# Optimization experiments

Hardware: AMD Instinct MI355X
Metric: run time of the kernel (lower is better)

## Reference

```python
import jax, jax.numpy as jnp
import numpy as np

DIM = 1024
D_STATE = 16
D_CONV = 4
EXPAND = 2
D_INNER = EXPAND * DIM          # 2048
DT_RANK = -(-DIM // 16)        # ceil(dim/16) = 64
BATCH = 2
SEQ = 1024


def activation_quant(x):
    # int8 fake-quant with STE, per-row scale (matches torch source incl. grad paths)
    scale = 127.0 / jnp.clip(jnp.max(jnp.abs(x), axis=-1, keepdims=True), 1e-5)
    s = x * scale
    q = jnp.clip(jnp.round(s), -128.0, 127.0)
    return (jax.lax.stop_gradient(q - s) + s) / scale


def weight_quant(w):
    # ternary quant {-1,0,1} with straight-through estimator (grad = identity)
    scale = jnp.clip(jnp.mean(jnp.abs(w)), 1e-5)
    wq = jnp.clip(jnp.round(w / scale), -1.0, 1.0)
    return w + jax.lax.stop_gradient(wq - w)


def bit_linear(x, w):
    # LayerNorm (no affine, eps=1e-5) -> act quant -> ternary-weight matmul
    mu = jnp.mean(x, axis=-1, keepdims=True)
    var = jnp.mean((x - mu) ** 2, axis=-1, keepdims=True)
    xn = (x - mu) * jax.lax.rsqrt(var + 1e-5)
    return activation_quant(xn) @ weight_quant(w).T


def rms_norm(x, w, eps=1e-6):
    return w * (x * jax.lax.rsqrt(jnp.mean(x * x, axis=-1, keepdims=True) + eps))


def selective_scan(x, delta, A, Bm, Cm, D, z):
    # x, delta: [b,l,d]; Bm, Cm: [b,l,n]; A: [d,n]; D: [d]; z: [b,l,d]
    def step(h, inp):
        x_t, d_t, B_t, C_t = inp              # [b,d],[b,d],[b,n],[b,n]
        dA = jnp.exp(d_t[:, :, None] * A)     # [b,d,n]
        h = dA * h + d_t[:, :, None] * B_t[:, None, :] * x_t[:, :, None]
        y = jnp.einsum('bdn,bn->bd', h, C_t)
        return h, y

    h0 = jnp.zeros((x.shape[0], A.shape[0], A.shape[1]), x.dtype)
    seq_first = lambda t: jnp.moveaxis(t, 1, 0)
    _, ys = jax.lax.scan(step, h0, (seq_first(x), seq_first(delta), seq_first(Bm), seq_first(Cm)))
    y = jnp.moveaxis(ys, 0, 1) + x * D
    return y * jax.nn.silu(z)


def mamba_forward(hidden_states, rms_w, in_proj_w, x_proj_w, out_proj_w,
                  conv_w, conv_b, dt_proj_w, dt_proj_b, A_log, D):
    b, l, _ = hidden_states.shape
    h = rms_norm(hidden_states, rms_w)
    xz = bit_linear(h, in_proj_w)                      # [b,l,2*d_inner]
    x, z = jnp.split(xz, 2, axis=-1)

    # depthwise causal conv1d + bias
    xc = jnp.moveaxis(x, 1, 2)                         # [b,d_inner,l]
    xc = jax.lax.conv_general_dilated(
        xc, conv_w, window_strides=(1,), padding=[(D_CONV - 1, 0)],
        feature_group_count=D_INNER, dimension_numbers=('NCH', 'OIH', 'NCH'))
    xc = xc + conv_b[None, :, None]
    x = jax.nn.silu(jnp.moveaxis(xc, 1, 2))            # [b,l,d_inner]

    x_dbl = bit_linear(x, x_proj_w)                    # [b,l,dt_rank+2*d_state]
    dt_low, Bm, Cm = jnp.split(x_dbl, [DT_RANK, DT_RANK + D_STATE], axis=-1)
    dt = dt_low @ dt_proj_w.T + dt_proj_b              # dt_proj (with bias)
    # source passes dt_bias=dt_proj.bias again into the fused scan with softplus
    delta = jax.nn.softplus(dt + dt_proj_b)
    A = -jnp.exp(A_log)

    y = selective_scan(x, delta, A, Bm, Cm, D, z)
    out = bit_linear(y, out_proj_w)
    return hidden_states + out


def setup_inputs() -> dict:
    key = jax.random.key(0)
    ks = jax.random.split(key, 8)
    return {
        'hidden_states': jax.random.normal(ks[0], (BATCH, SEQ, DIM), jnp.float32),
        'rms_w': jnp.ones((DIM,), jnp.float32),
        'in_proj_w': jax.random.normal(ks[1], (2 * D_INNER, DIM), jnp.float32) / np.float32(np.sqrt(DIM)),
        'x_proj_w': jax.random.normal(ks[2], (DT_RANK + 2 * D_STATE, D_INNER), jnp.float32) / np.float32(np.sqrt(D_INNER)),
        'out_proj_w': jax.random.normal(ks[3], (DIM, D_INNER), jnp.float32) / np.float32(np.sqrt(D_INNER)),
        'conv_w': jax.random.normal(ks[4], (D_INNER, 1, D_CONV), jnp.float32) * 0.2,
        'conv_b': jnp.zeros((D_INNER,), jnp.float32),
        'dt_proj_w': jax.random.normal(ks[5], (D_INNER, DT_RANK), jnp.float32) / np.float32(np.sqrt(DT_RANK)),
        'dt_proj_b': jax.random.normal(ks[6], (D_INNER,), jnp.float32) * 0.01,
        'A_log': jnp.log(jnp.tile(jnp.arange(1, D_STATE + 1, dtype=jnp.float32), (D_INNER, 1))),
        'D': jnp.ones((D_INNER,), jnp.float32),
    }


def reference(hidden_states, rms_w, in_proj_w, x_proj_w, out_proj_w,
              conv_w, conv_b, dt_proj_w, dt_proj_b, A_log, D):
    return mamba_forward(hidden_states, rms_w, in_proj_w, x_proj_w, out_proj_w,
                         conv_w, conv_b, dt_proj_w, dt_proj_b, A_log, D)
```

## Files before the change

kernel.cpp:

```cpp
#include <hip/hip_runtime.h>
#include <hip/hip_bf16.h>

#define BATCH 2
#define SEQ 1024
#define DIM 1024
#define DINNER 2048
#define NSTATE 16
#define DTRANK 64
#define NDBL 96
#define ROWS (BATCH*SEQ)
#define NC 32
#define TC 32
#define KSPLIT 8

#define N_IN_W  (4096*1024)
#define N_X_W   (NDBL*DINNER)
#define N_OUT_W (1024*2048)

typedef __attribute__((ext_vector_type(8))) short bf16x8;
typedef __attribute__((ext_vector_type(4))) float f32x4;

__device__ inline float wave_sum64(float v){
#pragma unroll
  for (int o=32;o>0;o>>=1) v += __shfl_xor(v,o,64);
  return v;
}
__device__ inline float wave_max64(float v){
#pragma unroll
  for (int o=32;o>0;o>>=1) v = fmaxf(v,__shfl_xor(v,o,64));
  return v;
}
__device__ inline float block_sum256(float v, float* sred){
  v = wave_sum64(v);
  if ((threadIdx.x&63)==0) sred[threadIdx.x>>6]=v;
  __syncthreads();
  float t = sred[0]+sred[1]+sred[2]+sred[3];
  __syncthreads();
  return t;
}
__device__ inline float block_max256(float v, float* sred){
  v = wave_max64(v);
  if ((threadIdx.x&63)==0) sred[threadIdx.x>>6]=v;
  __syncthreads();
  float t = fmaxf(fmaxf(sred[0],sred[1]),fmaxf(sred[2],sred[3]));
  __syncthreads();
  return t;
}

__global__ __launch_bounds__(256) void prelude_k(
    const float* __restrict__ w0, const float* __restrict__ w1,
    const float* __restrict__ w2, float* __restrict__ part,
    const float* __restrict__ hidden, const float* __restrict__ rmsw,
    __hip_bfloat16* __restrict__ q, float* __restrict__ rs,
    float* __restrict__ xdbl_zero)
{
  __shared__ float sred[4];
  const int bid = blockIdx.x, tid = threadIdx.x;
  if (bid < 1536){
    const int wsel = bid >> 9, bx = bid & 511;
    const float* w; int n;
    if (wsel==0){ w=w0; n=N_IN_W; }
    else if (wsel==1){ w=w1; n=N_X_W; }
    else { w=w2; n=N_OUT_W; }
    float s = 0.f;
    for (int i = bx*256 + tid; i < n; i += 512*256) s += fabsf(w[i]);
    s = block_sum256(s, sred);
    if (tid==0) part[wsel*512 + bx] = s;
    return;
  }
  if (bid < 3584){
    const int r = bid - 1536;
    const float* row = hidden + (size_t)r*1024;
    float v[4];
#pragma unroll
    for (int i=0;i<4;i++) v[i] = row[tid + i*256];
    float ss=0.f;
#pragma unroll
    for (int i=0;i<4;i++) ss += v[i]*v[i];
    ss = block_sum256(ss, sred);
    float f = rsqrtf(ss/1024.f + 1e-6f);
#pragma unroll
    for (int i=0;i<4;i++) v[i] *= f * rmsw[tid + i*256];
    float s=0.f;
#pragma unroll
    for (int i=0;i<4;i++) s += v[i];
    s = block_sum256(s, sred);
    const float mu = s/1024.f;
    float vs=0.f;
#pragma unroll
    for (int i=0;i<4;i++){ float d=v[i]-mu; vs += d*d; }
    vs = block_sum256(vs, sred);
    const float inv = rsqrtf(vs/1024.f + 1e-5f);
    float am=0.f;
#pragma unroll
    for (int i=0;i<4;i++){ v[i] = (v[i]-mu)*inv; am = fmaxf(am, fabsf(v[i])); }
    am = block_max256(am, sred);
    am = fmaxf(am, 1e-5f);
    const float scale = 127.f/am;
    if (tid==0) rs[r] = am*(1.f/127.f);
#pragma unroll
    for (int i=0;i<4;i++){
      float qv = fminf(fmaxf(rintf(v[i]*scale), -128.f), 127.f);
      q[(size_t)r*1024 + tid + i*256] = __float2bfloat16(qv);
    }
    return;
  }
  {
    const int idx = (bid - 3584)*256 + tid;
    ((float4*)xdbl_zero)[idx] = (float4){0.f,0.f,0.f,0.f};
  }
}

__device__ inline void tern4(const float* __restrict__ w, ushort* __restrict__ wq,
                             int i, float s){
  const float4 v = ((const float4*)w)[i];
  float q0 = fminf(fmaxf(rintf(v.x/s),-1.f),1.f);
  float q1 = fminf(fmaxf(rintf(v.y/s),-1.f),1.f);
  float q2 = fminf(fmaxf(rintf(v.z/s),-1.f),1.f);
  float q3 = fminf(fmaxf(rintf(v.w/s),-1.f),1.f);
  __hip_bfloat16 h0=__float2bfloat16(q0), h1=__float2bfloat16(q1);
  __hip_bfloat16 h2=__float2bfloat16(q2), h3=__float2bfloat16(q3);
  ushort4 o;
  o.x=*(ushort*)&h0; o.y=*(ushort*)&h1; o.z=*(ushort*)&h2; o.w=*(ushort*)&h3;
  ((ushort4*)wq)[i]=o;
}
__global__ __launch_bounds__(256) void ternarize3b_k(const float* __restrict__ w0,
    const float* __restrict__ w1, const float* __restrict__ w2,
    ushort* __restrict__ q0, ushort* __restrict__ q1, ushort* __restrict__ q2,
    const float* __restrict__ part){
  __shared__ float sred[4];
  float sc[3];
#pragma unroll
  for (int w=0; w<3; w++){
    float s = part[w*512 + threadIdx.x] + part[w*512 + threadIdx.x + 256];
    s = block_sum256(s, sred);
    const float c = (w==0)?(float)N_IN_W:((w==1)?(float)N_X_W:(float)N_OUT_W);
    sc[w] = fmaxf(s/c, 1e-5f);
  }
  const int NQ0 = N_IN_W/4, NQ1 = N_X_W/4, PQ1 = (128*2048 - N_X_W)/4, NQ2 = N_OUT_W/4;
  int i = blockIdx.x*256 + threadIdx.x;
  if (i < NQ0){ tern4(w0, q0, i, sc[0]); return; }
  i -= NQ0;
  if (i < NQ1){ tern4(w1, q1, i, sc[1]); return; }
  i -= NQ1;
  if (i < PQ1){ ((ushort4*)q1)[NQ1 + i] = (ushort4){0,0,0,0}; return; }
  i -= PQ1;
  if (i < NQ2){ tern4(w2, q2, i, sc[2]); }
}

__global__ __launch_bounds__(256) void conv_ln_quant_k(const float* __restrict__ x,
    const float* __restrict__ cw, const float* __restrict__ cb,
    float* __restrict__ xc, __hip_bfloat16* __restrict__ q, float* __restrict__ rs){
  __shared__ float sred[4];
  const int r = blockIdx.x, tid = threadIdx.x;
  const int t = r & (SEQ-1);
  float v[8];
#pragma unroll
  for (int i=0;i<8;i++){
    const int d = tid + i*256;
    const float4 w4 = ((const float4*)cw)[d];
    const float wj[4] = {w4.x, w4.y, w4.z, w4.w};
    float acc = cb[d];
#pragma unroll
    for (int j=0;j<4;j++){
      const int tt = t-3+j;
      if (tt>=0) acc += x[(size_t)(r-3+j)*DINNER + d]*wj[j];
    }
    acc = acc/(1.f+expf(-acc));
    xc[(size_t)r*DINNER + d] = acc;
    v[i] = acc;
  }
  float s=0.f;
#pragma unroll
  for (int i=0;i<8;i++) s += v[i];
  s = block_sum256(s, sred);
  const float mu = s/2048.f;
  float vs=0.f;
#pragma unroll
  for (int i=0;i<8;i++){ float d=v[i]-mu; vs += d*d; }
  vs = block_sum256(vs, sred);
  const float inv = rsqrtf(vs/2048.f + 1e-5f);
  float am=0.f;
#pragma unroll
  for (int i=0;i<8;i++){ v[i] = (v[i]-mu)*inv; am = fmaxf(am, fabsf(v[i])); }
  am = block_max256(am, sred);
  am = fmaxf(am, 1e-5f);
  const float scale = 127.f/am;
  if (tid==0) rs[r] = am*(1.f/127.f);
#pragma unroll
  for (int i=0;i<8;i++){
    float qv = fminf(fmaxf(rintf(v[i]*scale), -128.f), 127.f);
    q[(size_t)r*2048 + tid + i*256] = __float2bfloat16(qv);
  }
}

__global__ __launch_bounds__(256) void ln_quant8_k(const float* __restrict__ src,
    __hip_bfloat16* __restrict__ q, float* __restrict__ rs){
  __shared__ float sred[4];
  const int r = blockIdx.x, tid = threadIdx.x;
  const float* row = src + (size_t)r*2048;
  float v[8];
#pragma unroll
  for (int i=0;i<8;i++) v[i] = row[tid + i*256];
  float s=0.f;
#pragma unroll
  for (int i=0;i<8;i++) s += v[i];
  s = block_sum256(s, sred);
  const float mu = s/2048.f;
  float vs=0.f;
#pragma unroll
  for (int i=0;i<8;i++){ float d=v[i]-mu; vs += d*d; }
  vs = block_sum256(vs, sred);
  const float inv = rsqrtf(vs/2048.f + 1e-5f);
  float am=0.f;
#pragma unroll
  for (int i=0;i<8;i++){ v[i] = (v[i]-mu)*inv; am = fmaxf(am, fabsf(v[i])); }
  am = block_max256(am, sred);
  am = fmaxf(am, 1e-5f);
  const float scale = 127.f/am;
  if (tid==0) rs[r] = am*(1.f/127.f);
#pragma unroll
  for (int i=0;i<8;i++){
    float qv = fminf(fmaxf(rintf(v[i]*scale), -128.f), 127.f);
    q[(size_t)r*2048 + tid + i*256] = __float2bfloat16(qv);
  }
}

template<int BM, int BN, int MODE>
__global__ __launch_bounds__(256) void gemm2_k(
    const short* __restrict__ A, const short* __restrict__ Bw,
    const float* __restrict__ rs, int K, int Ksub, int ldc,
    float* __restrict__ out0, float* __restrict__ out1,
    const float* __restrict__ hid)
{
  constexpr int MF = BM/32;
  constexpr int NF = BN/32;
  constexpr int CA = BM/32;
  constexpr int CB = BN/32;
  __shared__ short lsA[BM*64];
  __shared__ short lsB[BN*64];
  const int tid = threadIdx.x;
  const int w = tid>>6, l = tid&63;
  const int m0 = blockIdx.x*BM, n0 = blockIdx.y*BN;
  const int wr = (w>>1)*(BM/2), wc = (w&1)*(BN/2);
  const int lr = l&15, g = l>>4;
  f32x4 acc[MF][NF];
#pragma unroll
  for (int m=0;m<MF;m++)
#pragma unroll
    for (int n=0;n<NF;n++) acc[m][n] = (f32x4){0.f,0.f,0.f,0.f};

  const size_t KB = (size_t)K*2;
  const char* Ag = (const char*)A + (size_t)m0*KB + (size_t)blockIdx.z*Ksub*2;
  const char* Bg = (const char*)Bw + (size_t)n0*KB + (size_t)blockIdx.z*Ksub*2;

  bf16x8 ra[CA], rb[CB];
#define LDG(kb)                                                                   \
  {                                                                               \
    _Pragma("unroll")                                                             \
    for (int c=0;c<CA;c++){ int o=c*4096+tid*16; int rw=o>>7, cl=o&127;           \
      ra[c] = *(const bf16x8*)(Ag + (size_t)rw*KB + (size_t)(kb)*2 + cl); }       \
    _Pragma("unroll")                                                             \
    for (int c=0;c<CB;c++){ int o=c*4096+tid*16; int rw=o>>7, cl=o&127;           \
      rb[c] = *(const bf16x8*)(Bg + (size_t)rw*KB + (size_t)(kb)*2 + cl); }       \
  }

  LDG(0);
  for (int kb=0; kb<Ksub; kb+=64){
    __syncthreads();
#pragma unroll
    for (int c=0;c<CA;c++){ int o=c*4096+tid*16; int rw=o>>7, sl=(o>>4)&7;
      *(bf16x8*)((char*)lsA + (rw<<7) + ((sl^(rw&7))<<4)) = ra[c]; }
#pragma unroll
    for (int c=0;c<CB;c++){ int o=c*4096+tid*16; int rw=o>>7, sl=(o>>4)&7;
      *(bf16x8*)((char*)lsB + (rw<<7) + ((sl^(rw&7))<<4)) = rb[c]; }
    __syncthreads();
    if (kb + 64 < Ksub) LDG(kb+64);
#pragma unroll
    for (int ks=0;ks<2;ks++){
      bf16x8 af[MF], bb[NF];
#pragma unroll
      for (int m=0;m<MF;m++){ int rw = wr + m*16 + lr;
        af[m] = *(const bf16x8*)((const char*)lsA + (rw<<7) + ((((ks<<2)+g)^(lr&7))<<4)); }
#pragma unroll
      for (int n=0;n<NF;n++){ int rw = wc + n*16 + lr;
        bb[n] = *(const bf16x8*)((const char*)lsB + (rw<<7) + ((((ks<<2)+g)^(lr&7))<<4)); }
#pragma unroll
      for (int m=0;m<MF;m++)
#pragma unroll
        for (int n=0;n<NF;n++)
          acc[m][n] = __builtin_amdgcn_mfma_f32_16x16x32_bf16(af[m], bb[n], acc[m][n], 0, 0, 0);
    }
  }
#undef LDG

#pragma unroll
  for (int m=0;m<MF;m++){
    const int rowb = m0 + wr + m*16 + g*4;
#pragma unroll
    for (int j=0;j<4;j++){
      const int row = rowb + j;
      const float rsv = (MODE==4) ? 1.f : rs[row];
#pragma unroll
      for (int n=0;n<NF;n++){
        const int col = n0 + wc + n*16 + lr;
        const float v = acc[m][n][j]*rsv;
        if (MODE==1){
          if (col < 2048) out0[(size_t)row*2048 + col] = v;
          else            out1[(size_t)row*2048 + (col-2048)] = v;
        } else if (MODE==2){
          const size_t o = (size_t)row*ldc + col;
          out0[o] = hid[o] + v;
        } else {
          if (col < NDBL) atomicAdd(&out0[(size_t)row*NDBL + col], v);
        }
      }
    }
  }
}

#define SXT_S 130
#define SW2_S 66
__global__ __launch_bounds__(256) void dt_delta2_k(const float* __restrict__ xdbl,
    const float* __restrict__ rs,
    const float* __restrict__ W, const float* __restrict__ bias, float* __restrict__ delta){
  __shared__ float sXT[64*SXT_S];
  __shared__ float sW2[64*SW2_S];
  const int tid = threadIdx.x;
  const int r0 = blockIdx.x*128, d0 = blockIdx.y*64;
#pragma unroll
  for (int qit=0;qit<8;qit++){
    const int f4 = qit*256 + tid;
    const int rr = f4>>4, k0 = (f4&15)<<2;
    const float rsv = rs[r0+rr];
    const float4 xv4 = *(const float4*)(xdbl + (size_t)(r0+rr)*NDBL + k0);
    sXT[(k0+0)*SXT_S + rr] = xv4.x*rsv;
    sXT[(k0+1)*SXT_S + rr] = xv4.y*rsv;
    sXT[(k0+2)*SXT_S + rr] = xv4.z*rsv;
    sXT[(k0+3)*SXT_S + rr] = xv4.w*rsv;
  }
#pragma unroll
  for (int qit=0;qit<4;qit++){
    const int f4 = qit*256 + tid;
    const int dd = f4>>4, k0 = (f4&15)<<2;
    const float4 wv4 = *(const float4*)(W + (size_t)(d0+dd)*64 + k0);
    sW2[(k0+0)*SW2_S + dd] = wv4.x;
    sW2[(k0+1)*SW2_S + dd] = wv4.y;
    sW2[(k0+2)*SW2_S + dd] = wv4.z;
    sW2[(k0+3)*SW2_S + dd] = wv4.w;
  }
  __syncthreads();
  const int tx = tid&15, ty = tid>>4;
  float acc[8][4];
#pragma unroll
  for (int i=0;i<8;i++)
#pragma unroll
    for (int j=0;j<4;j++) acc[i][j]=0.f;
  for (int k=0;k<64;k++){
    float xv[8], wv[4];
    *(float2*)&xv[0] = *(const float2*)&sXT[k*SXT_S + ty*8 + 0];
    *(float2*)&xv[2] = *(const float2*)&sXT[k*SXT_S + ty*8 + 2];
    *(float2*)&xv[4] = *(const float2*)&sXT[k*SXT_S + ty*8 + 4];
    *(float2*)&xv[6] = *(const float2*)&sXT[k*SXT_S + ty*8 + 6];
    *(float2*)&wv[0] = *(const float2*)&sW2[k*SW2_S + tx*4 + 0];
    *(float2*)&wv[2] = *(const float2*)&sW2[k*SW2_S + tx*4 + 2];
#pragma unroll
    for (int i=0;i<8;i++)
#pragma unroll
      for (int j=0;j<4;j++) acc[i][j] = fmaf(xv[i], wv[j], acc[i][j]);
  }
  const float4 b4 = *(const float4*)(bias + d0 + tx*4);
  const float b2[4] = {2.f*b4.x, 2.f*b4.y, 2.f*b4.z, 2.f*b4.w};
#pragma unroll
  for (int i=0;i<8;i++){
    const int row = r0 + ty*8 + i;
    float4 o;
    float* op = (float*)&o;
#pragma unroll
    for (int j=0;j<4;j++){
      const float xq = acc[i][j] + b2[j];
      op[j] = (xq>20.f) ? xq : log1pf(expf(xq));
    }
    *(float4*)(delta + (size_t)row*DINNER + d0 + tx*4) = o;
  }
}

__global__ __launch_bounds__(256) void scan1_k(const float* __restrict__ delta,
    const float* __restrict__ xc, const float* __restrict__ xdbl,
    const float* __restrict__ rs,
    const float* __restrict__ A_log, float* __restrict__ hloc, float* __restrict__ Ssum){
  __shared__ float sB[TC][16];
  const int tid = threadIdx.x;
  const int d = blockIdx.x*256 + tid;
  const int c = blockIdx.y, b = blockIdx.z;
  const int row0 = b*SEQ + c*TC;
  for (int i=tid;i<TC*16;i+=256){
    int t=i>>4, j=i&15;
    sB[t][j] = xdbl[(size_t)(row0+t)*NDBL + DTRANK + j] * rs[row0+t];
  }
  __syncthreads();
  float a[16];
  const f32x4* Ap = (const f32x4*)(A_log + (size_t)d*16);
#pragma unroll
  for (int q=0;q<4;q++){
    f32x4 av = Ap[q];
#pragma unroll
    for (int j=0;j<4;j++) a[q*4+j] = -__expf(av[j]);
  }
  float h[16];
#pragma unroll
  for (int n=0;n<16;n++) h[n]=0.f;
  float S = 0.f;
  float dl = delta[(size_t)row0*DINNER + d];
  float xv = xc[(size_t)row0*DINNER + d];
  for (int t=0;t<TC;t++){
    const float dlc=dl, xvc=xv;
    if (t<TC-1){
      dl = delta[(size_t)(row0+t+1)*DINNER + d];
      xv = xc[(size_t)(row0+t+1)*DINNER + d];
    }
    S += dlc;
    const float dx = dlc*xvc;
#pragma unroll
    for (int n=0;n<16;n++)
      h[n] = fmaf(__expf(dlc*a[n]), h[n], dx*sB[t][n]);
  }
  f32x4* hp = (f32x4*)(hloc + ((size_t)(b*NC+c)*DINNER + d)*16);
#pragma unroll
  for (int q=0;q<4;q++){
    f32x4 hv;
#pragma unroll
    for (int j=0;j<4;j++) hv[j]=h[q*4+j];
    hp[q]=hv;
  }
  Ssum[(size_t)(b*NC+c)*DINNER + d] = S;
}

__global__ __launch_bounds__(256) void scan2_k(const float* __restrict__ A_log,
    const float* __restrict__ Ssum, float* __restrict__ hloc){
  const int idx = blockIdx.x*256 + threadIdx.x;
  const int n = idx&15, d = (idx>>4)&(DINNER-1), b = idx>>15;
  const float a = -__expf(A_log[(size_t)d*16+n]);
  float hin = 0.f;
  for (int c=0;c<NC;c++){
    const size_t o = ((size_t)(b*NC+c)*DINNER + d)*16 + n;
    const float t = hloc[o];
    hloc[o] = hin;
    hin = fmaf(__expf(a*Ssum[(size_t)(b*NC+c)*DINNER + d]), hin, t);
  }
}

__global__ __launch_bounds__(256) void scan3_k(const float* __restrict__ delta,
    const float* __restrict__ xc, const float* __restrict__ xdbl,
    const float* __restrict__ rs,
    const float* __restrict__ A_log, const float* __restrict__ Dp,
    const float* __restrict__ hloc, float* __restrict__ zy){
  __shared__ float sBC[TC][32];
  const int tid = threadIdx.x;
  const int d = blockIdx.x*256 + tid;
  const int c = blockIdx.y, b = blockIdx.z;
  const int row0 = b*SEQ + c*TC;
  for (int i=tid;i<TC*32;i+=256){
    int t=i>>5, j=i&31;
    sBC[t][j] = xdbl[(size_t)(row0+t)*NDBL + DTRANK + j] * rs[row0+t];
  }
  __syncthreads();
  float a[16];
  const f32x4* Ap = (const f32x4*)(A_log + (size_t)d*16);
#pragma unroll
  for (int q=0;q<4;q++){
    f32x4 av = Ap[q];
#pragma unroll
    for (int j=0;j<4;j++) a[q*4+j] = -__expf(av[j]);
  }
  float h[16];
  const f32x4* hp = (const f32x4*)(hloc + ((size_t)(b*NC+c)*DINNER + d)*16);
#pragma unroll
  for (int q=0;q<4;q++){
    f32x4 hv = hp[q];
#pragma unroll
    for (int j=0;j<4;j++) h[q*4+j]=hv[j];
  }
  const float Dv = Dp[d];
  float dl = delta[(size_t)row0*DINNER + d];
  float xv = xc[(size_t)row0*DINNER + d];
  float zv = zy[(size_t)row0*DINNER + d];
  for (int t=0;t<TC;t++){
    const float dlc=dl, xvc=xv, zvc=zv;
    if (t<TC-1){
      dl = delta[(size_t)(row0+t+1)*DINNER + d];
      xv = xc[(size_t)(row0+t+1)*DINNER + d];
      zv = zy[(size_t)(row0+t+1)*DINNER + d];
    }
    const float dx = dlc*xvc;
    float p = 0.f;
#pragma unroll
    for (int n=0;n<16;n++){
      h[n] = fmaf(__expf(dlc*a[n]), h[n], dx*sBC[t][n]);
      p = fmaf(h[n], sBC[t][16+n], p);
    }
    float y = p + xvc*Dv;
    y *= zvc/(1.f+__expf(-zvc));
    zy[(size_t)(row0+t)*DINNER + d] = y;
  }
}

extern "C" void kernel_launch(void* const* d_in, const int* in_sizes, int n_in,
                              void* d_out, int out_size, void* d_ws, size_t ws_size,
                              hipStream_t stream){
  (void)in_sizes; (void)n_in; (void)out_size; (void)ws_size;
  const float* hidden    = (const float*)d_in[0];
  const float* rms_w     = (const float*)d_in[1];
  const float* in_proj_w = (const float*)d_in[2];
  const float* x_proj_w  = (const float*)d_in[3];
  const float* out_proj_w= (const float*)d_in[4];
  const float* conv_w    = (const float*)d_in[5];
  const float* conv_b    = (const float*)d_in[6];
  const float* dt_proj_w = (const float*)d_in[7];
  const float* dt_proj_b = (const float*)d_in[8];
  const float* A_log     = (const float*)d_in[9];
  const float* Dp        = (const float*)d_in[10];

  char* ws = (char*)d_ws; size_t off = 0;
  auto alloc = [&](size_t b)->void* { void* p = ws + off; off += (b + 255) & ~(size_t)255; return p; };
  float* part3 = (float*)alloc(3*512*4);
  float* RS    = (float*)alloc((size_t)ROWS*4);
  __hip_bfloat16* WQin  = (__hip_bfloat16*)alloc((size_t)4096*1024*2);
  __hip_bfloat16* WQx   = (__hip_bfloat16*)alloc((size_t)128*2048*2);
  __hip_bfloat16* WQout = (__hip_bfloat16*)alloc((size_t)1024*2048*2);
  __hip_bfloat16* QA    = (__hip_bfloat16*)alloc((size_t)ROWS*2048*2);
  float* XBUF  = (float*)alloc((size_t)ROWS*DINNER*4);
  float* ZBUF  = (float*)alloc((size_t)ROWS*DINNER*4);
  float* XC    = (float*)alloc((size_t)ROWS*DINNER*4);
  float* XDBL  = (float*)alloc((size_t)ROWS*NDBL*4);
  float* HLOC  = (float*)alloc((size_t)BATCH*NC*DINNER*16*4);
  float* SSUM  = (float*)alloc((size_t)BATCH*NC*DINNER*4);

  prelude_k<<<3776,256,0,stream>>>(in_proj_w, x_proj_w, out_proj_w, part3,
                                   hidden, rms_w, QA, RS, XDBL);
  {
    const int totq = N_IN_W/4 + 128*2048/4 + N_OUT_W/4;
    ternarize3b_k<<<(totq+255)/256,256,0,stream>>>(in_proj_w, x_proj_w, out_proj_w,
        (ushort*)WQin, (ushort*)WQx, (ushort*)WQout, part3);
  }
  gemm2_k<128,128,1><<<dim3(ROWS/128, 4096/128, 1),256,0,stream>>>((const short*)QA,
      (const short*)WQin, RS, DIM, DIM, 0, XBUF, ZBUF, nullptr);
  conv_ln_quant_k<<<ROWS,256,0,stream>>>(XBUF, conv_w, conv_b, XC, QA, RS);
  gemm2_k<64,128,4><<<dim3(ROWS/64, 1, KSPLIT),256,0,stream>>>((const short*)QA,
      (const short*)WQx, nullptr, DINNER, DINNER/KSPLIT, NDBL, XDBL, nullptr, nullptr);
  dt_delta2_k<<<dim3(ROWS/128, DINNER/64),256,0,stream>>>(XDBL, RS, dt_proj_w, dt_proj_b, XBUF);
  scan1_k<<<dim3(DINNER/256, NC, BATCH),256,0,stream>>>(XBUF, XC, XDBL, RS, A_log, HLOC, SSUM);
  scan2_k<<<(BATCH*DINNER*16)/256,256,0,stream>>>(A_log, SSUM, HLOC);
  scan3_k<<<dim3(DINNER/256, NC, BATCH),256,0,stream>>>(XBUF, XC, XDBL, RS, A_log, Dp, HLOC, ZBUF);
  ln_quant8_k<<<ROWS,256,0,stream>>>(ZBUF, QA, RS);
  gemm2_k<64,64,2><<<dim3(ROWS/64, 1024/64, 1),256,0,stream>>>((const short*)QA,
      (const short*)WQout, RS, DINNER, DINNER, DIM, (float*)d_out, nullptr, hidden);
}
```

Before: 180.1 us.

## Fuse conv, dt projection and softplus into scan kernels, drop XC/delta buffers

Removes the separate dt_delta kernel and the materialized conv output: both scan passes now recompute the causal conv+SiLU from the raw x buffer and compute delta by a 64-wide dot product against a per-thread register copy of dt_proj weights staged through LDS. This cuts global writes and reads of two ROWSxDINNER float buffers and one launch. In exchange the conv, projection and softplus are computed twice (scan1 and scan3), register pressure rises with 64 weight registers, and each block loads a 64KB weight tile into LDS, which limits occupancy.

Result: slower. 205.6 us (+14.1%).

```diff
diff --git a/kernel.cpp b/kernel.cpp
--- a/kernel.cpp
+++ b/kernel.cpp
@@ -12,6 +12,7 @@
 #define NC 32
 #define TC 32
 #define KSPLIT 8
+#define SWT_P 257
 
 #define N_IN_W  (4096*1024)
 #define N_X_W   (NDBL*DINNER)
@@ -150,7 +151,7 @@
 
 __global__ __launch_bounds__(256) void conv_ln_quant_k(const float* __restrict__ x,
     const float* __restrict__ cw, const float* __restrict__ cb,
-    float* __restrict__ xc, __hip_bfloat16* __restrict__ q, float* __restrict__ rs){
+    __hip_bfloat16* __restrict__ q, float* __restrict__ rs){
   __shared__ float sred[4];
   const int r = blockIdx.x, tid = threadIdx.x;
   const int t = r & (SEQ-1);
@@ -167,7 +168,6 @@
       if (tt>=0) acc += x[(size_t)(r-3+j)*DINNER + d]*wj[j];
     }
     acc = acc/(1.f+expf(-acc));
-    xc[(size_t)r*DINNER + d] = acc;
     v[i] = acc;
   }
   float s=0.f;
@@ -319,111 +319,95 @@
   }
 }
 
-#define SXT_S 130
-#define SW2_S 66
-__global__ __launch_bounds__(256) void dt_delta2_k(const float* __restrict__ xdbl,
-    const float* __restrict__ rs,
-    const float* __restrict__ W, const float* __restrict__ bias, float* __restrict__ delta){
-  __shared__ float sXT[64*SXT_S];
-  __shared__ float sW2[64*SW2_S];
+__global__ __launch_bounds__(256,2) void scan1f_k(const float* __restrict__ xbuf,
+    const float* __restrict__ xdbl, const float* __restrict__ rs,
+    const float* __restrict__ cw, const float* __restrict__ cb,
+    const float* __restrict__ dtW, const float* __restrict__ dtb,
+    const float* __restrict__ A_log, float* __restrict__ hloc, float* __restrict__ Ssum){
+  __shared__ float sWT[64*SWT_P];
+  __shared__ float sX[TC*64];
+  __shared__ float sB[TC*16];
   const int tid = threadIdx.x;
-  const int r0 = blockIdx.x*128, d0 = blockIdx.y*64;
-#pragma unroll
-  for (int qit=0;qit<8;qit++){
-    const int f4 = qit*256 + tid;
-    const int rr = f4>>4, k0 = (f4&15)<<2;
-    const float rsv = rs[r0+rr];
-    const float4 xv4 = *(const float4*)(xdbl + (size_t)(r0+rr)*NDBL + k0);
-    sXT[(k0+0)*SXT_S + rr] = xv4.x*rsv;
-    sXT[(k0+1)*SXT_S + rr] = xv4.y*rsv;
-    sXT[(k0+2)*SXT_S + rr] = xv4.z*rsv;
-    sXT[(k0+3)*SXT_S + rr] = xv4.w*rsv;
-  }
-#pragma unroll
-  for (int qit=0;qit<4;qit++){
-    const int f4 = qit*256 + tid;
-    const int dd = f4>>4, k0 = (f4&15)<<2;
-    const float4 wv4 = *(const float4*)(W + (size_t)(d0+dd)*64 + k0);
-    sW2[(k0+0)*SW2_S + dd] = wv4.x;
-    sW2[(k0+1)*SW2_S + dd] = wv4.y;
-    sW2[(k0+2)*SW2_S + dd] = wv4.z;
-    sW2[(k0+3)*SW2_S + dd] = wv4.w;
-  }
-  __syncthreads();
-  const int tx = tid&15, ty = tid>>4;
-  float acc[8][4];
-#pragma unroll
-  for (int i=0;i<8;i++)
-#pragma unroll
-    for (int j=0;j<4;j++) acc[i][j]=0.f;
-  for (int k=0;k<64;k++){
-    float xv[8], wv[4];
-    *(float2*)&xv[0] = *(const float2*)&sXT[k*SXT_S + ty*8 + 0];
-    *(float2*)&xv[2] = *(const float2*)&sXT[k*SXT_S + ty*8 + 2];
-    *(float2*)&xv[4] = *(const float2*)&sXT[k*SXT_S + ty*8 + 4];
-    *(float2*)&xv[6] = *(const float2*)&sXT[k*SXT_S + ty*8 + 6];
-    *(float2*)&wv[0] = *(const float2*)&sW2[k*SW2_S + tx*4 + 0];
-    *(float2*)&wv[2] = *(const float2*)&sW2[k*SW2_S + tx*4 + 2];
-#pragma unroll
-    for (int i=0;i<8;i++)
-#pragma unroll
-      for (int j=0;j<4;j++) acc[i][j] = fmaf(xv[i], wv[j], acc[i][j]);
-  }
-  const float4 b4 = *(const float4*)(bias + d0 + tx*4);
-  const float b2[4] = {2.f*b4.x, 2.f*b4.y, 2.f*b4.z, 2.f*b4.w};
-#pragma unroll
-  for (int i=0;i<8;i++){
-    const int row = r0 + ty*8 + i;
-    float4 o;
-    float* op = (float*)&o;
-#pragma unroll
-    for (int j=0;j<4;j++){
-      const float xq = acc[i][j] + b2[j];
-      op[j] = (xq>20.f) ? xq : log1pf(expf(xq));
-    }
-    *(float4*)(delta + (size_t)row*DINNER + d0 + tx*4) = o;
-  }
-}
-
-__global__ __launch_bounds__(256) void scan1_k(const float* __restrict__ delta,
-    const float* __restrict__ xc, const float* __restrict__ xdbl,
-    const float* __restrict__ rs,
-    const float* __restrict__ A_log, float* __restrict__ hloc, float* __restrict__ Ssum){
-  __shared__ float sB[TC][16];
-  const int tid = threadIdx.x;
-  const int d = blockIdx.x*256 + tid;
+  const int d0 = blockIdx.x*256;
+  const int d  = d0 + tid;
   const int c = blockIdx.y, b = blockIdx.z;
   const int row0 = b*SEQ + c*TC;
-  for (int i=tid;i<TC*16;i+=256){
-    int t=i>>4, j=i&15;
-    sB[t][j] = xdbl[(size_t)(row0+t)*NDBL + DTRANK + j] * rs[row0+t];
+  for (int i = tid; i < 4096; i += 256){
+    const int dd = i >> 4, k4 = (i & 15) << 2;
+    const float4 w4 = *(const float4*)(dtW + (size_t)(d0+dd)*64 + k4);
+    sWT[(k4+0)*SWT_P + dd] = w4.x;
+    sWT[(k4+1)*SWT_P + dd] = w4.y;
+    sWT[(k4+2)*SWT_P + dd] = w4.z;
+    sWT[(k4+3)*SWT_P + dd] = w4.w;
+  }
+  for (int i = tid; i < TC*24; i += 256){
+    const int t = i/24, k4 = (i - t*24)*4;
+    const float rsv = rs[row0+t];
+    const float4 v = *(const float4*)(xdbl + (size_t)(row0+t)*NDBL + k4);
+    if (k4 < 64){
+      sX[t*64+k4+0]=v.x*rsv; sX[t*64+k4+1]=v.y*rsv;
+      sX[t*64+k4+2]=v.z*rsv; sX[t*64+k4+3]=v.w*rsv;
+    } else if (k4 < 80){
+      const int j = k4-64;
+      sB[t*16+j+0]=v.x*rsv; sB[t*16+j+1]=v.y*rsv;
+      sB[t*16+j+2]=v.z*rsv; sB[t*16+j+3]=v.w*rsv;
+    }
   }
   __syncthreads();
+  float wreg[64];
+#pragma unroll
+  for (int k=0;k<64;k++) wreg[k] = sWT[k*SWT_P + tid];
   float a[16];
-  const f32x4* Ap = (const f32x4*)(A_log + (size_t)d*16);
-#pragma unroll
-  for (int q=0;q<4;q++){
-    f32x4 av = Ap[q];
-#pragma unroll
-    for (int j=0;j<4;j++) a[q*4+j] = -__expf(av[j]);
-  }
+  {
+    const f32x4* Ap = (const f32x4*)(A_log + (size_t)d*16);
+#pragma unroll
+    for (int q=0;q<4;q++){
+      f32x4 av = Ap[q];
+#pragma unroll
+      for (int j=0;j<4;j++) a[q*4+j] = -__expf(av[j]);
+    }
+  }
+  const float4 w4 = ((const float4*)cw)[d];
+  const float cbv = cb[d];
+  const float b2 = 2.f*dtb[d];
+  float xm3=0.f, xm2=0.f, xm1=0.f;
+  if (c > 0){
+    xm3 = xbuf[(size_t)(row0-3)*DINNER + d];
+    xm2 = xbuf[(size_t)(row0-2)*DINNER + d];
+    xm1 = xbuf[(size_t)(row0-1)*DINNER + d];
+  }
+  float xcur = xbuf[(size_t)row0*DINNER + d];
   float h[16];
 #pragma unroll
   for (int n=0;n<16;n++) h[n]=0.f;
   float S = 0.f;
-  float dl = delta[(size_t)row0*DINNER + d];
-  float xv = xc[(size_t)row0*DINNER + d];
   for (int t=0;t<TC;t++){
-    const float dlc=dl, xvc=xv;
-    if (t<TC-1){
-      dl = delta[(size_t)(row0+t+1)*DINNER + d];
-      xv = xc[(size_t)(row0+t+1)*DINNER + d];
-    }
+    float xnext = 0.f;
+    if (t < TC-1) xnext = xbuf[(size_t)(row0+t+1)*DINNER + d];
+    const int tseq = c*TC + t;
+    float acc = cbv;
+    if (tseq-3 >= 0) acc += xm3*w4.x;
+    if (tseq-2 >= 0) acc += xm2*w4.y;
+    if (tseq-1 >= 0) acc += xm1*w4.z;
+    acc += xcur*w4.w;
+    const float xvc = acc/(1.f+expf(-acc));
+    float dacc = 0.f;
+#pragma unroll
+    for (int k4=0;k4<16;k4++){
+      const float4 xf = *(const float4*)&sX[t*64 + k4*4];
+      dacc = fmaf(xf.x, wreg[k4*4+0], dacc);
+      dacc = fmaf(xf.y, wreg[k4*4+1], dacc);
+      dacc = fmaf(xf.z, wreg[k4*4+2], dacc);
+      dacc = fmaf(xf.w, wreg[k4*4+3], dacc);
+    }
+    const float xq = dacc + b2;
+    const float dlc = (xq>20.f) ? xq : log1pf(expf(xq));
     S += dlc;
     const float dx = dlc*xvc;
 #pragma unroll
     for (int n=0;n<16;n++)
-      h[n] = fmaf(__expf(dlc*a[n]), h[n], dx*sB[t][n]);
+      h[n] = fmaf(__expf(dlc*a[n]), h[n], dx*sB[t*16+n]);
+    xm3=xm2; xm2=xm1; xm1=xcur; xcur=xnext;
   }
   f32x4* hp = (f32x4*)(hloc + ((size_t)(b*NC+c)*DINNER + d)*16);
 #pragma unroll
@@ -450,58 +434,113 @@
   }
 }
 
-__global__ __launch_bounds__(256) void scan3_k(const float* __restrict__ delta,
-    const float* __restrict__ xc, const float* __restrict__ xdbl,
-    const float* __restrict__ rs,
+__global__ __launch_bounds__(256,2) void scan3f_k(const float* __restrict__ xbuf,
+    const float* __restrict__ xdbl, const float* __restrict__ rs,
+    const float* __restrict__ cw, const float* __restrict__ cb,
+    const float* __restrict__ dtW, const float* __restrict__ dtb,
     const float* __restrict__ A_log, const float* __restrict__ Dp,
     const float* __restrict__ hloc, float* __restrict__ zy){
-  __shared__ float sBC[TC][32];
+  __shared__ float sWT[64*SWT_P];
+  __shared__ float sX[TC*64];
+  __shared__ float sBC[TC*32];
   const int tid = threadIdx.x;
-  const int d = blockIdx.x*256 + tid;
+  const int d0 = blockIdx.x*256;
+  const int d  = d0 + tid;
   const int c = blockIdx.y, b = blockIdx.z;
   const int row0 = b*SEQ + c*TC;
-  for (int i=tid;i<TC*32;i+=256){
-    int t=i>>5, j=i&31;
-    sBC[t][j] = xdbl[(size_t)(row0+t)*NDBL + DTRANK + j] * rs[row0+t];
+  for (int i = tid; i < 4096; i += 256){
+    const int dd = i >> 4, k4 = (i & 15) << 2;
+    const float4 w4 = *(const float4*)(dtW + (size_t)(d0+dd)*64 + k4);
+    sWT[(k4+0)*SWT_P + dd] = w4.x;
+    sWT[(k4+1)*SWT_P + dd] = w4.y;
+    sWT[(k4+2)*SWT_P + dd] = w4.z;
+    sWT[(k4+3)*SWT_P + dd] = w4.w;
+  }
+  for (int i = tid; i < TC*24; i += 256){
+    const int t = i/24, k4 = (i - t*24)*4;
+    const float rsv = rs[row0+t];
+    const float4 v = *(const float4*)(xdbl + (size_t)(row0+t)*NDBL + k4);
+    if (k4 < 64){
+      sX[t*64+k4+0]=v.x*rsv; sX[t*64+k4+1]=v.y*rsv;
+      sX[t*64+k4+2]=v.z*rsv; sX[t*64+k4+3]=v.w*rsv;
+    } else {
+      const int j = k4-64;
+      sBC[t*32+j+0]=v.x*rsv; sBC[t*32+j+1]=v.y*rsv;
+      sBC[t*32+j+2]=v.z*rsv; sBC[t*32+j+3]=v.w*rsv;
+    }
   }
   __syncthreads();
+  float wreg[64];
+#pragma unroll
+  for (int k=0;k<64;k++) wreg[k] = sWT[k*SWT_P + tid];
   float a[16];
-  const f32x4* Ap = (const f32x4*)(A_log + (size_t)d*16);
-#pragma unroll
-  for (int q=0;q<4;q++){
-    f32x4 av = Ap[q];
-#pragma unroll
-    for (int j=0;j<4;j++) a[q*4+j] = -__expf(av[j]);
-  }
+  {
+    const f32x4* Ap = (const f32x4*)(A_log + (size_t)d*16);
+#pragma unroll
+    for (int q=0;q<4;q++){
+      f32x4 av = Ap[q];
+#pragma unroll
+      for (int j=0;j<4;j++) a[q*4+j] = -__expf(av[j]);
+    }
+  }
+  const float4 w4 = ((const float4*)cw)[d];
+  const float cbv = cb[d];
+  const float b2 = 2.f*dtb[d];
+  const float Dv = Dp[d];
   float h[16];
-  const f32x4* hp = (const f32x4*)(hloc + ((size_t)(b*NC+c)*DINNER + d)*16);
-#pragma unroll
-  for (int q=0;q<4;q++){
-    f32x4 hv = hp[q];
-#pragma unroll
-    for (int j=0;j<4;j++) h[q*4+j]=hv[j];
-  }
-  const float Dv = Dp[d];
-  float dl = delta[(size_t)row0*DINNER + d];
-  float xv = xc[(size_t)row0*DINNER + d];
+  {
+    const f32x4* hp = (const f32x4*)(hloc + ((size_t)(b*NC+c)*DINNER + d)*16);
+#pragma unroll
+    for (int q=0;q<4;q++){
+      f32x4 hv = hp[q];
+#pragma unroll
+      for (int j=0;j<4;j++) h[q*4+j]=hv[j];
+    }
+  }
+  float xm3=0.f, xm2=0.f, xm1=0.f;
+  if (c > 0){
+    xm3 = xbuf[(size_t)(row0-3)*DINNER + d];
+    xm2 = xbuf[(size_t)(row0-2)*DINNER + d];
+    xm1 = xbuf[(size_t)(row0-1)*DINNER + d];
+  }
+  float xcur = xbuf[(size_t)row0*DINNER + d];
   float zv = zy[(size_t)row0*DINNER + d];
   for (int t=0;t<TC;t++){
-    const float dlc=dl, xvc=xv, zvc=zv;
-    if (t<TC-1){
-      dl = delta[(size_t)(row0+t+1)*DINNER + d];
-      xv = xc[(size_t)(row0+t+1)*DINNER + d];
-      zv = zy[(size_t)(row0+t+1)*DINNER + d];
-    }
+    float xnext = 0.f, znext = 0.f;
+    if (t < TC-1){
+      xnext = xbuf[(size_t)(row0+t+1)*DINNER + d];
+      znext = zy[(size_t)(row0+t+1)*DINNER + d];
+    }
+    const int tseq = c*TC + t;
+    float acc = cbv;
+    if (tseq-3 >= 0) acc += xm3*w4.x;
+    if (tseq-2 >= 0) acc += xm2*w4.y;
+    if (tseq-1 >= 0) acc += xm1*w4.z;
+    acc += xcur*w4.w;
+    const float xvc = acc/(1.f+expf(-acc));
+    float dacc = 0.f;
+#pragma unroll
+    for (int k4=0;k4<16;k4++){
+      const float4 xf = *(const float4*)&sX[t*64 + k4*4];
+      dacc = fmaf(xf.x, wreg[k4*4+0], dacc);
+      dacc = fmaf(xf.y, wreg[k4*4+1], dacc);
+      dacc = fmaf(xf.z, wreg[k4*4+2], dacc);
+      dacc = fmaf(xf.w, wreg[k4*4+3], dacc);
+    }
+    const float xq = dacc + b2;
+    const float dlc = (xq>20.f) ? xq : log1pf(expf(xq));
     const float dx = dlc*xvc;
     float p = 0.f;
 #pragma unroll
     for (int n=0;n<16;n++){
-      h[n] = fmaf(__expf(dlc*a[n]), h[n], dx*sBC[t][n]);
-      p = fmaf(h[n], sBC[t][16+n], p);
-    }
+      h[n] = fmaf(__expf(dlc*a[n]), h[n], dx*sBC[t*32+n]);
+      p = fmaf(h[n], sBC[t*32+16+n], p);
+    }
+    const float zvc = zv;
     float y = p + xvc*Dv;
     y *= zvc/(1.f+__expf(-zvc));
     zy[(size_t)(row0+t)*DINNER + d] = y;
+    xm3=xm2; xm2=xm1; xm1=xcur; xcur=xnext; zv=znext;
   }
 }
 
@@ -531,7 +570,6 @@
   __hip_bfloat16* QA    = (__hip_bfloat16*)alloc((size_t)ROWS*2048*2);
   float* XBUF  = (float*)alloc((size_t)ROWS*DINNER*4);
   float* ZBUF  = (float*)alloc((size_t)ROWS*DINNER*4);
-  float* XC    = (float*)alloc((size_t)ROWS*DINNER*4);
   float* XDBL  = (float*)alloc((size_t)ROWS*NDBL*4);
   float* HLOC  = (float*)alloc((size_t)BATCH*NC*DINNER*16*4);
   float* SSUM  = (float*)alloc((size_t)BATCH*NC*DINNER*4);
@@ -545,13 +583,14 @@
   }
   gemm2_k<128,128,1><<<dim3(ROWS/128, 4096/128, 1),256,0,stream>>>((const short*)QA,
       (const short*)WQin, RS, DIM, DIM, 0, XBUF, ZBUF, nullptr);
-  conv_ln_quant_k<<<ROWS,256,0,stream>>>(XBUF, conv_w, conv_b, XC, QA, RS);
+  conv_ln_quant_k<<<ROWS,256,0,stream>>>(XBUF, conv_w, conv_b, QA, RS);
   gemm2_k<64,128,4><<<dim3(ROWS/64, 1, KSPLIT),256,0,stream>>>((const short*)QA,
       (const short*)WQx, nullptr, DINNER, DINNER/KSPLIT, NDBL, XDBL, nullptr, nullptr);
-  dt_delta2_k<<<dim3(ROWS/128, DINNER/64),256,0,stream>>>(XDBL, RS, dt_proj_w, dt_proj_b, XBUF);
-  scan1_k<<<dim3(DINNER/256, NC, BATCH),256,0,stream>>>(XBUF, XC, XDBL, RS, A_log, HLOC, SSUM);
+  scan1f_k<<<dim3(DINNER/256, NC, BATCH),256,0,stream>>>(XBUF, XDBL, RS,
+      conv_w, conv_b, dt_proj_w, dt_proj_b, A_log, HLOC, SSUM);
   scan2_k<<<(BATCH*DINNER*16)/256,256,0,stream>>>(A_log, SSUM, HLOC);
-  scan3_k<<<dim3(DINNER/256, NC, BATCH),256,0,stream>>>(XBUF, XC, XDBL, RS, A_log, Dp, HLOC, ZBUF);
+  scan3f_k<<<dim3(DINNER/256, NC, BATCH),256,0,stream>>>(XBUF, XDBL, RS,
+      conv_w, conv_b, dt_proj_w, dt_proj_b, A_log, Dp, HLOC, ZBUF);
   ln_quant8_k<<<ROWS,256,0,stream>>>(ZBUF, QA, RS);
   gemm2_k<64,64,2><<<dim3(ROWS/64, 1024/64, 1),256,0,stream>>>((const short*)QA,
       (const short*)WQout, RS, DINNER, DINNER, DIM, (float*)d_out, nullptr, hidden);
```

## Recompute causal conv+SiLU inside scan kernels and halve scan chunk length

Applied to the files above, without the earlier changes.

The conv+SiLU output is no longer written to a separate buffer. Both scan passes recompute it on the fly from the pre-conv x buffer using a rolling 4-tap window, which drops a 16 MB write and two 16 MB reads. Delta now gets its own buffer instead of overwriting the x buffer. The scan chunk length is halved and the chunk count doubled, giving more blocks for parallelism but a longer serial chain in scan2 and more HLOC traffic. The cost is extra exp and divide work per element in both scan kernels.

After: 187.6 us. +4.1%, slower.

```diff
diff --git a/kernel.cpp b/kernel.cpp
--- a/kernel.cpp
+++ b/kernel.cpp
@@ -9,8 +9,8 @@
 #define DTRANK 64
 #define NDBL 96
 #define ROWS (BATCH*SEQ)
-#define NC 32
-#define TC 32
+#define NC 64
+#define TC 16
 #define KSPLIT 8
 
 #define N_IN_W  (4096*1024)
@@ -150,7 +150,7 @@
 
 __global__ __launch_bounds__(256) void conv_ln_quant_k(const float* __restrict__ x,
     const float* __restrict__ cw, const float* __restrict__ cb,
-    float* __restrict__ xc, __hip_bfloat16* __restrict__ q, float* __restrict__ rs){
+    __hip_bfloat16* __restrict__ q, float* __restrict__ rs){
   __shared__ float sred[4];
   const int r = blockIdx.x, tid = threadIdx.x;
   const int t = r & (SEQ-1);
@@ -167,7 +167,6 @@
       if (tt>=0) acc += x[(size_t)(r-3+j)*DINNER + d]*wj[j];
     }
     acc = acc/(1.f+expf(-acc));
-    xc[(size_t)r*DINNER + d] = acc;
     v[i] = acc;
   }
   float s=0.f;
@@ -385,45 +384,61 @@
   }
 }
 
-__global__ __launch_bounds__(256) void scan1_k(const float* __restrict__ delta,
-    const float* __restrict__ xc, const float* __restrict__ xdbl,
-    const float* __restrict__ rs,
-    const float* __restrict__ A_log, float* __restrict__ hloc, float* __restrict__ Ssum){
-  __shared__ float sB[TC][16];
+__global__ __launch_bounds__(256) void scan1f_k(const float* __restrict__ xbuf,
+    const float* __restrict__ delta, const float* __restrict__ xdbl,
+    const float* __restrict__ rs, const float* __restrict__ cw,
+    const float* __restrict__ cb, const float* __restrict__ A_log,
+    float* __restrict__ hloc, float* __restrict__ Ssum){
+  __shared__ float sB[TC*16];
   const int tid = threadIdx.x;
   const int d = blockIdx.x*256 + tid;
   const int c = blockIdx.y, b = blockIdx.z;
   const int row0 = b*SEQ + c*TC;
-  for (int i=tid;i<TC*16;i+=256){
-    int t=i>>4, j=i&15;
-    sB[t][j] = xdbl[(size_t)(row0+t)*NDBL + DTRANK + j] * rs[row0+t];
+  {
+    const int t = tid>>4, j = tid&15;
+    sB[t*16+j] = xdbl[(size_t)(row0+t)*NDBL + DTRANK + j] * rs[row0+t];
   }
   __syncthreads();
   float a[16];
-  const f32x4* Ap = (const f32x4*)(A_log + (size_t)d*16);
-#pragma unroll
-  for (int q=0;q<4;q++){
-    f32x4 av = Ap[q];
-#pragma unroll
-    for (int j=0;j<4;j++) a[q*4+j] = -__expf(av[j]);
-  }
+  {
+    const f32x4* Ap = (const f32x4*)(A_log + (size_t)d*16);
+#pragma unroll
+    for (int q=0;q<4;q++){
+      f32x4 av = Ap[q];
+#pragma unroll
+      for (int j=0;j<4;j++) a[q*4+j] = -__expf(av[j]);
+    }
+  }
+  const float4 w4 = ((const float4*)cw)[d];
+  const float cbv = cb[d];
+  float xm3=0.f, xm2=0.f, xm1=0.f;
+  if (c > 0){
+    xm3 = xbuf[(size_t)(row0-3)*DINNER + d];
+    xm2 = xbuf[(size_t)(row0-2)*DINNER + d];
+    xm1 = xbuf[(size_t)(row0-1)*DINNER + d];
+  }
+  float xcur = xbuf[(size_t)row0*DINNER + d];
   float h[16];
 #pragma unroll
   for (int n=0;n<16;n++) h[n]=0.f;
   float S = 0.f;
-  float dl = delta[(size_t)row0*DINNER + d];
-  float xv = xc[(size_t)row0*DINNER + d];
   for (int t=0;t<TC;t++){
-    const float dlc=dl, xvc=xv;
-    if (t<TC-1){
-      dl = delta[(size_t)(row0+t+1)*DINNER + d];
-      xv = xc[(size_t)(row0+t+1)*DINNER + d];
-    }
+    float xnext = 0.f;
+    if (t < TC-1) xnext = xbuf[(size_t)(row0+t+1)*DINNER + d];
+    const float dlc = delta[(size_t)(row0+t)*DINNER + d];
+    const int tseq = c*TC + t;
+    float acc = cbv;
+    if (tseq-3 >= 0) acc += xm3*w4.x;
+    if (tseq-2 >= 0) acc += xm2*w4.y;
+    if (tseq-1 >= 0) acc += xm1*w4.z;
+    acc += xcur*w4.w;
+    const float xvc = acc/(1.f+expf(-acc));
     S += dlc;
     const float dx = dlc*xvc;
 #pragma unroll
     for (int n=0;n<16;n++)
-      h[n] = fmaf(__expf(dlc*a[n]), h[n], dx*sB[t][n]);
+      h[n] = fmaf(__expf(dlc*a[n]), h[n], dx*sB[t*16+n]);
+    xm3=xm2; xm2=xm1; xm1=xcur; xcur=xnext;
   }
   f32x4* hp = (f32x4*)(hloc + ((size_t)(b*NC+c)*DINNER + d)*16);
 #pragma unroll
@@ -450,58 +465,81 @@
   }
 }
 
-__global__ __launch_bounds__(256) void scan3_k(const float* __restrict__ delta,
-    const float* __restrict__ xc, const float* __restrict__ xdbl,
-    const float* __restrict__ rs,
-    const float* __restrict__ A_log, const float* __restrict__ Dp,
-    const float* __restrict__ hloc, float* __restrict__ zy){
-  __shared__ float sBC[TC][32];
+__global__ __launch_bounds__(256) void scan3f_k(const float* __restrict__ xbuf,
+    const float* __restrict__ delta, const float* __restrict__ xdbl,
+    const float* __restrict__ rs, const float* __restrict__ cw,
+    const float* __restrict__ cb, const float* __restrict__ A_log,
+    const float* __restrict__ Dp, const float* __restrict__ hloc,
+    float* __restrict__ zy){
+  __shared__ float sBC[TC*32];
   const int tid = threadIdx.x;
   const int d = blockIdx.x*256 + tid;
   const int c = blockIdx.y, b = blockIdx.z;
   const int row0 = b*SEQ + c*TC;
-  for (int i=tid;i<TC*32;i+=256){
-    int t=i>>5, j=i&31;
-    sBC[t][j] = xdbl[(size_t)(row0+t)*NDBL + DTRANK + j] * rs[row0+t];
+#pragma unroll
+  for (int i0=0;i0<2;i0++){
+    const int i = i0*256 + tid;
+    const int t = i>>5, j = i&31;
+    sBC[t*32+j] = xdbl[(size_t)(row0+t)*NDBL + DTRANK + j] * rs[row0+t];
   }
   __syncthreads();
   float a[16];
-  const f32x4* Ap = (const f32x4*)(A_log + (size_t)d*16);
-#pragma unroll
-  for (int q=0;q<4;q++){
-    f32x4 av = Ap[q];
-#pragma unroll
-    for (int j=0;j<4;j++) a[q*4+j] = -__expf(av[j]);
-  }
+  {
+    const f32x4* Ap = (const f32x4*)(A_log + (size_t)d*16);
+#pragma unroll
+    for (int q=0;q<4;q++){
+      f32x4 av = Ap[q];
+#pragma unroll
+      for (int j=0;j<4;j++) a[q*4+j] = -__expf(av[j]);
+    }
+  }
+  const float4 w4 = ((const float4*)cw)[d];
+  const float cbv = cb[d];
+  const float Dv = Dp[d];
   float h[16];
-  const f32x4* hp = (const f32x4*)(hloc + ((size_t)(b*NC+c)*DINNER + d)*16);
-#pragma unroll
-  for (int q=0;q<4;q++){
-    f32x4 hv = hp[q];
-#pragma unroll
-    for (int j=0;j<4;j++) h[q*4+j]=hv[j];
-  }
-  const float Dv = Dp[d];
-  float dl = delta[(size_t)row0*DINNER + d];
-  float xv = xc[(size_t)row0*DINNER + d];
+  {
+    const f32x4* hp = (const f32x4*)(hloc + ((size_t)(b*NC+c)*DINNER + d)*16);
+#pragma unroll
+    for (int q=0;q<4;q++){
+      f32x4 hv = hp[q];
+#pragma unroll
+      for (int j=0;j<4;j++) h[q*4+j]=hv[j];
+    }
+  }
+  float xm3=0.f, xm2=0.f, xm1=0.f;
+  if (c > 0){
+    xm3 = xbuf[(size_t)(row0-3)*DINNER + d];
+    xm2 = xbuf[(size_t)(row0-2)*DINNER + d];
+    xm1 = xbuf[(size_t)(row0-1)*DINNER + d];
+  }
+  float xcur = xbuf[(size_t)row0*DINNER + d];
   float zv = zy[(size_t)row0*DINNER + d];
   for (int t=0;t<TC;t++){
-    const float dlc=dl, xvc=xv, zvc=zv;
-    if (t<TC-1){
-      dl = delta[(size_t)(row0+t+1)*DINNER + d];
-      xv = xc[(size_t)(row0+t+1)*DINNER + d];
-      zv = zy[(size_t)(row0+t+1)*DINNER + d];
-    }
+    float xnext = 0.f, znext = 0.f;
+    if (t < TC-1){
+      xnext = xbuf[(size_t)(row0+t+1)*DINNER + d];
+      znext = zy[(size_t)(row0+t+1)*DINNER + d];
+    }
+    const float dlc = delta[(size_t)(row0+t)*DINNER + d];
+    const int tseq = c*TC + t;
+    float acc = cbv;
+    if (tseq-3 >= 0) acc += xm3*w4.x;
+    if (tseq-2 >= 0) acc += xm2*w4.y;
+    if (tseq-1 >= 0) acc += xm1*w4.z;
+    acc += xcur*w4.w;
+    const float xvc = acc/(1.f+expf(-acc));
     const float dx = dlc*xvc;
     float p = 0.f;
 #pragma unroll
     for (int n=0;n<16;n++){
-      h[n] = fmaf(__expf(dlc*a[n]), h[n], dx*sBC[t][n]);
-      p = fmaf(h[n], sBC[t][16+n], p);
-    }
+      h[n] = fmaf(__expf(dlc*a[n]), h[n], dx*sBC[t*32+n]);
+      p = fmaf(h[n], sBC[t*32+16+n], p);
+    }
+    const float zvc = zv;
     float y = p + xvc*Dv;
     y *= zvc/(1.f+__expf(-zvc));
     zy[(size_t)(row0+t)*DINNER + d] = y;
+    xm3=xm2; xm2=xm1; xm1=xcur; xcur=xnext; zv=znext;
   }
 }
 
@@ -531,7 +569,7 @@
   __hip_bfloat16* QA    = (__hip_bfloat16*)alloc((size_t)ROWS*2048*2);
   float* XBUF  = (float*)alloc((size_t)ROWS*DINNER*4);
   float* ZBUF  = (float*)alloc((size_t)ROWS*DINNER*4);
-  float* XC    = (float*)alloc((size_t)ROWS*DINNER*4);
+  float* DELTA = (float*)alloc((size_t)ROWS*DINNER*4);
   float* XDBL  = (float*)alloc((size_t)ROWS*NDBL*4);
   float* HLOC  = (float*)alloc((size_t)BATCH*NC*DINNER*16*4);
   float* SSUM  = (float*)alloc((size_t)BATCH*NC*DINNER*4);
@@ -545,13 +583,15 @@
   }
   gemm2_k<128,128,1><<<dim3(ROWS/128, 4096/128, 1),256,0,stream>>>((const short*)QA,
       (const short*)WQin, RS, DIM, DIM, 0, XBUF, ZBUF, nullptr);
-  conv_ln_quant_k<<<ROWS,256,0,stream>>>(XBUF, conv_w, conv_b, XC, QA, RS);
+  conv_ln_quant_k<<<ROWS,256,0,stream>>>(XBUF, conv_w, conv_b, QA, RS);
   gemm2_k<64,128,4><<<dim3(ROWS/64, 1, KSPLIT),256,0,stream>>>((const short*)QA,
       (const short*)WQx, nullptr, DINNER, DINNER/KSPLIT, NDBL, XDBL, nullptr, nullptr);
-  dt_delta2_k<<<dim3(ROWS/128, DINNER/64),256,0,stream>>>(XDBL, RS, dt_proj_w, dt_proj_b, XBUF);
-  scan1_k<<<dim3(DINNER/256, NC, BATCH),256,0,stream>>>(XBUF, XC, XDBL, RS, A_log, HLOC, SSUM);
+  dt_delta2_k<<<dim3(ROWS/128, DINNER/64),256,0,stream>>>(XDBL, RS, dt_proj_w, dt_proj_b, DELTA);
+  scan1f_k<<<dim3(DINNER/256, NC, BATCH),256,0,stream>>>(XBUF, DELTA, XDBL, RS,
+      conv_w, conv_b, A_log, HLOC, SSUM);
   scan2_k<<<(BATCH*DINNER*16)/256,256,0,stream>>>(A_log, SSUM, HLOC);
-  scan3_k<<<dim3(DINNER/256, NC, BATCH),256,0,stream>>>(XBUF, XC, XDBL, RS, A_log, Dp, HLOC, ZBUF);
+  scan3f_k<<<dim3(DINNER/256, NC, BATCH),256,0,stream>>>(XBUF, DELTA, XDBL, RS,
+      conv_w, conv_b, A_log, Dp, HLOC, ZBUF);
   ln_quant8_k<<<ROWS,256,0,stream>>>(ZBUF, QA, RS);
   gemm2_k<64,64,2><<<dim3(ROWS/64, 1024/64, 1),256,0,stream>>>((const short*)QA,
       (const short*)WQout, RS, DINNER, DINNER, DIM, (float*)d_out, nullptr, hidden);
```
